# Kernel optimization log

Hardware: AMD Instinct MI355X
Metric: run time of the kernel (lower is better)

## Reference

```python
import jax, jax.numpy as jnp
import numpy as np

E = 2        # expan_att_chans
HEADS = 16   # num_chans * expan_att_chans


def _gconv1x1(x, w, b, groups):
    # Grouped 1x1 conv. x: [B, Cin, H, W]; w: [Cout, Cin//groups]; b: [Cout].
    # Output channel layout matches torch: group-major (c_group * gout + o).
    B, Cin, H, W = x.shape
    Cout = w.shape[0]
    gin, gout = Cin // groups, Cout // groups
    y = jnp.einsum('bgip,goi->bgop',
                   x.reshape(B, groups, gin, H * W),
                   w.reshape(groups, gout, gin))
    return y.reshape(B, Cout, H, W) + b[None, :, None, None]


def _l2norm(x, eps=1e-12):
    # F.normalize(dim=-1): x / max(||x||_2, eps)
    n = jnp.sqrt(jnp.sum(x * x, axis=-1, keepdims=True))
    return x / jnp.maximum(n, eps)


def setup_inputs() -> dict:
    key = jax.random.key(0)
    ks = jax.random.split(key, 12)
    B, C, H, W = 8, 128, 128, 128
    s = 0.05  # small init (module uses xavier gain=0.01)
    f32 = jnp.float32
    return {
        'x': jax.random.normal(ks[0], (B, C, H, W), f32),
        'to': jax.random.normal(ks[1], (B, C, H, W), f32),
        't': jnp.ones((1, HEADS, 1, 1), f32),
        # rgb qkv chain (fusion): C -> 2EC -> EC -> EC, all groups=C
        'w_r1': (jax.random.normal(ks[2], (C * E * 2, 1), f32) * s),
        'b_r1': jnp.zeros((C * E * 2,), f32),
        'w_r2': (jax.random.normal(ks[3], (C * E, 2 * E), f32) * s),
        'b_r2': jnp.zeros((C * E,), f32),
        'w_r3': (jax.random.normal(ks[4], (C * E, E), f32) * s),
        'b_r3': jnp.zeros((C * E,), f32),
        # text kv chain: C -> 2EC -> EC -> 2EC, all groups=C
        'w_t1': (jax.random.normal(ks[5], (C * E * 2, 1), f32) * s),
        'b_t1': jnp.zeros((C * E * 2,), f32),
        'w_t2': (jax.random.normal(ks[6], (C * E, 2 * E), f32) * s),
        'b_t2': jnp.zeros((C * E,), f32),
        'w_t3': (jax.random.normal(ks[7], (C * E * 2, E), f32) * s),
        'b_t3': jnp.zeros((C * E * 2,), f32),
        # fusion conv: Conv2d(E*C -> C, k=3, stride=1, pad=1) + LeakyReLU(0.2)
        'w_f': (jax.random.normal(ks[8], (C, C * E, 3, 3), f32) * 0.02),
        'b_f': jnp.zeros((C,), f32),
    }


def reference(x, to, t, w_r1, b_r1, w_r2, b_r2, w_r3, b_r3,
              w_t1, b_t1, w_t2, b_t2, w_t3, b_t3, w_f, b_f):
    B, C, H, W = x.shape
    Cexp = E * C
    d = Cexp // HEADS  # per-head channel dim
    HW = H * W

    # grouped 1x1 conv chains producing Q (from rgb) and K,V (from text)
    q = _gconv1x1(_gconv1x1(_gconv1x1(x, w_r1, b_r1, C), w_r2, b_r2, C), w_r3, b_r3, C)      # [B, EC, H, W]
    kv = _gconv1x1(_gconv1x1(_gconv1x1(to, w_t1, b_t1, C), w_t2, b_t2, C), w_t3, b_t3, C)    # [B, 2EC, H, W]

    # Rearrange 'B (C E) H W -> B E C H W' then view as [B, heads, d, HW]
    q = q.reshape(B, C, E, HW).transpose(0, 2, 1, 3).reshape(B, HEADS, d, HW)
    kv = kv.reshape(B, C, 2 * E, HW).transpose(0, 2, 1, 3)  # [B, 2E, C, HW]
    k = kv[:, :E].reshape(B, HEADS, d, HW)
    v = kv[:, E:].reshape(B, HEADS, d, HW)

    # channel (transposed) attention with L2-normalized Q,K and learned temperature
    qn, kn = _l2norm(q), _l2norm(k)
    attn = jax.nn.softmax(jnp.einsum('bhdp,bhep->bhde', qn, kn) * t, axis=-1)  # [B, H, d, d]
    xo = jnp.einsum('bhde,bhep->bhdp', attn, v)  # [B, heads, d, HW]

    # rearrange 'B C X (H W) -> B (X C) H W' with C=heads, X=d  (d-major, head-minor)
    xo = xo.transpose(0, 2, 1, 3).reshape(B, Cexp, H, W)

    # group_fus: 3x3 conv (stride 1, pad 1) + LeakyReLU(0.2), residual add
    y = jax.lax.conv_general_dilated(
        xo, w_f, window_strides=(1, 1), padding=((1, 1), (1, 1)),
        dimension_numbers=('NCHW', 'OIHW', 'NCHW'))
    y = jax.nn.leaky_relu(y + b_f[None, :, None, None], negative_slope=0.2)
    return x + y
```

## Files before the change

kernel.cpp:

```cpp
#include <hip/hip_runtime.h>
#include <math.h>

#define B_  8
#define C_  128
#define H_  128
#define W_  128
#define HW_ 16384

#define OFF_MPART 0
#define OFF_SPART 262144
#define OFF_M     327680
#define OFF_S     344064
#define OFF_WV    348160
#define OFF_CST   380928
#define OFF_T     382976
#define OFF_WEFF  392192
#define OFF_T2F   982016
#define T2_ROW    16640
#define T2_BATCH  2163200
#define WS_NEED   (982016ull * 4ull + 34611200ull)

typedef __attribute__((ext_vector_type(8))) short short8;
typedef __attribute__((ext_vector_type(4))) float f32x4;

__device__ __forceinline__ unsigned short f2bf(float f) {
  unsigned u = __float_as_uint(f);
  u += 0x7fffu + ((u >> 16) & 1u);
  return (unsigned short)(u >> 16);
}

__device__ __forceinline__ f32x4 mfma16(short8 a, short8 b, f32x4 c) {
  return __builtin_amdgcn_mfma_f32_16x16x32_bf16(a, b, c, 0, 0, 0);
}

__device__ __forceinline__ void gl16(const void* g, void* l) {
  const unsigned loff = (unsigned)(unsigned long long)l;
  __builtin_amdgcn_global_load_lds(
      (const __attribute__((address_space(1))) void*)g,
      (__attribute__((address_space(3))) void*)loff, 16, 0, 0);
}

__global__ __launch_bounds__(256) void k_gram(const float* __restrict__ x,
                                              const float* __restrict__ to,
                                              float* __restrict__ ws) {
  const int bid = blockIdx.x;
  const int ps  = bid & 15;
  const int blk = (bid >> 4) & 7;
  const int b   = bid >> 7;
  const int tid = threadIdx.x;
  const int w = tid >> 6, l = tid & 63;
  const int lm = l & 15, lh = l >> 4;
  const int c0 = blk * 16;

  const float* xc = x  + ((size_t)b * C_ + c0 + lm) * HW_;
  const float* tc = to + ((size_t)b * C_ + c0 + lm) * HW_;
  const int p0 = ps * 1024 + w * 256 + lh * 8;

  f32x4 acc = (f32x4)0.f;
  float sx = 0.f, sxx = 0.f, st = 0.f, stt = 0.f;
#pragma unroll
  for (int it = 0; it < 8; ++it) {
    const int p = p0 + it * 32;
    const f32x4 xa = *(const f32x4*)(xc + p);
    const f32x4 xb = *(const f32x4*)(xc + p + 4);
    const f32x4 ta = *(const f32x4*)(tc + p);
    const f32x4 tb = *(const f32x4*)(tc + p + 4);
    short8 xf, tf;
#pragma unroll
    for (int e = 0; e < 4; ++e) {
      xf[e]     = (short)f2bf(xa[e]);
      xf[4 + e] = (short)f2bf(xb[e]);
      tf[e]     = (short)f2bf(ta[e]);
      tf[4 + e] = (short)f2bf(tb[e]);
      sx += xa[e] + xb[e];
      sxx = fmaf(xa[e], xa[e], fmaf(xb[e], xb[e], sxx));
      st += ta[e] + tb[e];
      stt = fmaf(ta[e], ta[e], fmaf(tb[e], tb[e], stt));
    }
    acc = mfma16(xf, tf, acc);
  }

  sx  += __shfl_xor(sx, 16);  sx  += __shfl_xor(sx, 32);
  sxx += __shfl_xor(sxx, 16); sxx += __shfl_xor(sxx, 32);
  st  += __shfl_xor(st, 16);  st  += __shfl_xor(st, 32);
  stt += __shfl_xor(stt, 16); stt += __shfl_xor(stt, 32);

  __shared__ float smM[4][256];
  __shared__ float smS[4][4][16];
#pragma unroll
  for (int r = 0; r < 4; ++r)
    smM[w][(lh * 4 + r) * 16 + lm] = acc[r];
  if (l < 16) {
    smS[w][0][lm] = sx;  smS[w][1][lm] = sxx;
    smS[w][2][lm] = st;  smS[w][3][lm] = stt;
  }
  __syncthreads();

  {
    const float s = smM[0][tid & 255] + smM[1][tid & 255]
                  + smM[2][tid & 255] + smM[3][tid & 255];
    ws[OFF_MPART + (size_t)((b * 8 + blk) * 16 + ps) * 256 + tid] = s;
  }
  if (tid < 64) {
    const int kind = tid >> 4, ch = tid & 15;
    const float s = smS[0][kind][ch] + smS[1][kind][ch]
                  + smS[2][kind][ch] + smS[3][kind][ch];
    ws[OFF_SPART + (size_t)kind * 16384 + (size_t)(b * C_ + c0 + ch) * 16 + ps] = s;
  }
}

__global__ __launch_bounds__(256) void k_redB(float* __restrict__ ws) {
  const int gid = blockIdx.x * 256 + threadIdx.x;
  if (gid < 16384) {
    const float* mp = ws + OFF_MPART + (size_t)(gid >> 8) * 4096 + (gid & 255);
    float s = 0.f;
#pragma unroll
    for (int kc = 0; kc < 16; ++kc) s += mp[kc * 256];
    ws[OFF_M + gid] = s;
  } else {
    const int sidx = gid - 16384;
    const float* sp = ws + OFF_SPART + (size_t)sidx * 16;
    float s = 0.f;
#pragma unroll
    for (int kc = 0; kc < 16; ++kc) s += sp[kc];
    ws[OFF_S + sidx] = s;
  }
}

__global__ __launch_bounds__(256) void k_zero(unsigned short* __restrict__ t2) {
  const int b = blockIdx.x >> 1, r = blockIdx.x & 1;
  unsigned short* row = t2 + (size_t)b * T2_BATCH + (size_t)(r ? 129 : 0) * T2_ROW;
  const short8 z = {0,0,0,0,0,0,0,0};
  for (int idx = threadIdx.x; idx < 2080; idx += 256)
    *(short8*)(row + (size_t)idx * 8) = z;
}

__global__ __launch_bounds__(256) void k_tr(const float* __restrict__ to,
                                            unsigned short* __restrict__ t2) {
  const int d  = blockIdx.x;
  const int xh = d & 1;
  const int y  = (d >> 1) & 127;
  const int b  = d >> 8;
  const int tid = threadIdx.x;
  __shared__ char lds[64 * 256];

  const int x0 = xh * 64;
  const int xq = tid & 15;
  const int cg = tid >> 4;
  const float* srcb = to + ((size_t)b * C_ + cg * 8) * HW_ + (size_t)y * W_ + x0 + xq * 4;
#pragma unroll
  for (int k = 0; k < 8; ++k) {
    const f32x4 v = *(const f32x4*)(srcb + (size_t)k * HW_);
    const int c = cg * 8 + k;
#pragma unroll
    for (int e = 0; e < 4; ++e) {
      const int xl = xq * 4 + e;
      const int boff = xl * 256 + ((2 * c) ^ ((xl & 7) << 4));
      *(unsigned short*)(lds + boff) = f2bf(v[e]);
    }
  }
  __syncthreads();

  unsigned short* rowbase = t2 + (size_t)b * T2_BATCH + (size_t)(y + 1) * T2_ROW;
#pragma unroll
  for (int i = 0; i < 4; ++i) {
    const int xx = tid >> 2;
    const int cs = (tid & 3) + i * 4;
    short8 val = *(short8*)(lds + xx * 256 + ((cs * 16) ^ ((xx & 7) << 4)));
    *(short8*)(rowbase + (size_t)(x0 + xx + 1) * 128 + cs * 8) = val;
  }
  if (tid < 16) {
    short8 z = {0,0,0,0,0,0,0,0};
    if (xh == 0) *(short8*)(rowbase + tid * 8) = z;
    else         *(short8*)(rowbase + (size_t)129 * 128 + tid * 8) = z;
  }
}

__global__ __launch_bounds__(256) void k_attn(const float* __restrict__ t,
    const float* __restrict__ w_r1, const float* __restrict__ b_r1,
    const float* __restrict__ w_r2, const float* __restrict__ b_r2,
    const float* __restrict__ w_r3, const float* __restrict__ b_r3,
    const float* __restrict__ w_t1, const float* __restrict__ b_t1,
    const float* __restrict__ w_t2, const float* __restrict__ b_t2,
    const float* __restrict__ w_t3, const float* __restrict__ b_t3,
    float* __restrict__ ws) {
  const int b = blockIdx.x;
  const int tid = threadIdx.x;
  __shared__ float aQ[256], bQ[256], aK[256], bK[256], aV[256], bV[256];
  __shared__ float rks[256], kAs[256], kBs[256], stos[256];

  if (tid < 128) {
    const int g = tid;
    float A1[4], B1[4], A2[2], B2[2];
#pragma unroll
    for (int j = 0; j < 4; ++j) { A1[j] = w_r1[g * 4 + j]; B1[j] = b_r1[g * 4 + j]; }
#pragma unroll
    for (int i = 0; i < 2; ++i) {
      A2[i] = 0.f; B2[i] = b_r2[g * 2 + i];
#pragma unroll
      for (int j = 0; j < 4; ++j) {
        const float w = w_r2[(g * 2 + i) * 4 + j];
        A2[i] = fmaf(w, A1[j], A2[i]); B2[i] = fmaf(w, B1[j], B2[i]);
      }
    }
#pragma unroll
    for (int o = 0; o < 2; ++o) {
      float a = 0.f, bb = b_r3[g * 2 + o];
#pragma unroll
      for (int i = 0; i < 2; ++i) {
        const float w = w_r3[(g * 2 + o) * 2 + i];
        a = fmaf(w, A2[i], a); bb = fmaf(w, B2[i], bb);
      }
      aQ[g * 2 + o] = a; bQ[g * 2 + o] = bb;
    }
#pragma unroll
    for (int j = 0; j < 4; ++j) { A1[j] = w_t1[g * 4 + j]; B1[j] = b_t1[g * 4 + j]; }
#pragma unroll
    for (int i = 0; i < 2; ++i) {
      A2[i] = 0.f; B2[i] = b_t2[g * 2 + i];
#pragma unroll
      for (int j = 0; j < 4; ++j) {
        const float w = w_t2[(g * 2 + i) * 4 + j];
        A2[i] = fmaf(w, A1[j], A2[i]); B2[i] = fmaf(w, B1[j], B2[i]);
      }
    }
#pragma unroll
    for (int o = 0; o < 4; ++o) {
      float a = 0.f, bb = b_t3[g * 4 + o];
#pragma unroll
      for (int i = 0; i < 2; ++i) {
        const float w = w_t3[(g * 4 + o) * 2 + i];
        a = fmaf(w, A2[i], a); bb = fmaf(w, B2[i], bb);
      }
      if (o < 2) { aK[g * 2 + o] = a; bK[g * 2 + o] = bb; }
      else       { aV[g * 2 + (o - 2)] = a; bV[g * 2 + (o - 2)] = bb; }
    }
  }
  __syncthreads();

  const float* S   = ws + OFF_S;
  const float* Sx  = S;
  const float* Sxx = S + 1024;
  const float* Sto = S + 2048;
  const float* Stt = S + 3072;

  {
    const int h = tid >> 4, e = h >> 3, blk = h & 7, c0 = blk * 16;
    const int g = c0 + (tid & 15);
    const float a = aK[g * 2 + e], bb = bK[g * 2 + e];
    const float s2 = a * a * Stt[b * C_ + g] + 2.f * a * bb * Sto[b * C_ + g]
                   + bb * bb * 16384.f;
    rks[tid] = 1.f / fmaxf(sqrtf(fmaxf(s2, 0.f)), 1e-12f);
    kAs[tid] = a; kBs[tid] = bb;
    stos[tid] = Sto[b * C_ + g];
  }
  __syncthreads();

  {
    const int h = tid >> 4, i = tid & 15, e = h >> 3, blk = h & 7, c0 = blk * 16;
    const int gi = c0 + i;
    const float gA = aQ[gi * 2 + e], gB = bQ[gi * 2 + e];
    const float sxi = Sx[b * C_ + gi];
    const float q2 = gA * gA * Sxx[b * C_ + gi] + 2.f * gA * gB * sxi
                   + gB * gB * 16384.f;
    const float rnq = 1.f / fmaxf(sqrtf(fmaxf(q2, 0.f)), 1e-12f);
    const float tt = t[h];
    const float* Mrow = ws + OFF_M + (size_t)(b * 8 + blk) * 256 + i * 16;

    float lg[16];
    float mx = -1e30f;
#pragma unroll
    for (int j = 0; j < 16; ++j) {
      const float s = gA * kAs[h * 16 + j] * Mrow[j]
                    + gA * kBs[h * 16 + j] * sxi
                    + gB * kAs[h * 16 + j] * stos[h * 16 + j]
                    + gB * kBs[h * 16 + j] * 16384.f;
      const float l = tt * s * rnq * rks[h * 16 + j];
      lg[j] = l;
      mx = fmaxf(mx, l);
    }
    float den = 0.f;
#pragma unroll
    for (int j = 0; j < 16; ++j) { const float ev = expf(lg[j] - mx); lg[j] = ev; den += ev; }
    const float inv = 1.f / den;
    float cs = 0.f;
    float* WVp = ws + OFF_WV + (size_t)(b * 16 + h) * 256 + i * 16;
#pragma unroll
    for (int j = 0; j < 16; ++j) {
      const float aa = lg[j] * inv;
      const int gj = c0 + j;
      WVp[j] = aa * aV[gj * 2 + e];
      cs = fmaf(aa, bV[gj * 2 + e], cs);
    }
    ws[OFF_CST + b * 256 + i * 16 + h] = cs;
  }
}

__global__ __launch_bounds__(128) void k_weff(const float* __restrict__ w_f,
                                              float* __restrict__ ws) {
  const int b = blockIdx.x >> 7, oc = blockIdx.x & 127;
  const int c = threadIdx.x, blk = c >> 4, j = c & 15;
  const float* WVb = ws + OFF_WV;
  float acc[9];
#pragma unroll
  for (int k = 0; k < 9; ++k) acc[k] = 0.f;
#pragma unroll
  for (int e = 0; e < 2; ++e) {
    const int h = e * 8 + blk;
#pragma unroll
    for (int i = 0; i < 16; ++i) {
      const float coef = WVb[((size_t)(b * 16 + h) * 16 + i) * 16 + j];
      const float* wf = w_f + (size_t)(oc * 256 + i * 16 + h) * 9;
#pragma unroll
      for (int k = 0; k < 9; ++k) acc[k] = fmaf(wf[k], coef, acc[k]);
    }
  }
  unsigned short* wb16 = (unsigned short*)(ws + OFF_WEFF);
#pragma unroll
  for (int k = 0; k < 9; ++k)
    wb16[(((size_t)(b * 9 + k)) * 128 + oc) * 128 + c] = f2bf(acc[k]);

  __shared__ float tp[9][128];
  float tl[9];
#pragma unroll
  for (int k = 0; k < 9; ++k) tl[k] = 0.f;
  const float* cst = ws + OFF_CST + b * 256;
  for (int cc = c; cc < 256; cc += 128) {
    const float cv = cst[cc];
    const float* wf = w_f + (size_t)(oc * 256 + cc) * 9;
#pragma unroll
    for (int k = 0; k < 9; ++k) tl[k] = fmaf(wf[k], cv, tl[k]);
  }
#pragma unroll
  for (int k = 0; k < 9; ++k) tp[k][c] = tl[k];
  __syncthreads();
  for (int s = 64; s > 0; s >>= 1) {
    if (c < s) {
#pragma unroll
      for (int k = 0; k < 9; ++k) tp[k][c] += tp[k][c + s];
    }
    __syncthreads();
  }
  if (c < 9) ws[OFF_T + ((size_t)b * 128 + oc) * 9 + c] = tp[c][0];
}

__global__ __launch_bounds__(256, 2) void k_conv(const float* __restrict__ xin,
                                                 const float* __restrict__ b_f,
                                                 const float* __restrict__ ws,
                                                 const unsigned short* __restrict__ t2,
                                                 float* __restrict__ out) {
  const int d = blockIdx.x;
  const int b = d & 7;
  const int y = d >> 3;
  const int tid = threadIdx.x;

  __shared__ unsigned short As[2][128 * 64];
  __shared__ unsigned short Bs[2][128 * 64];

  const unsigned short* wb = (const unsigned short*)(ws + OFF_WEFF)
      + (size_t)b * 9 * 16384;
  const unsigned short* t2y = t2 + (size_t)b * T2_BATCH + (size_t)y * T2_ROW;

  const int l = tid & 63;
  const int lm = l & 15, lh = l >> 4;
  const int wv = tid >> 6;
  const int oc0w = (wv & 1) * 64;
  const int px0w = (wv >> 1) * 64;

  const int trow0 = tid >> 3, tci0 = tid & 7;
  const unsigned udstw = (unsigned)((tid & ~63) * 16);

#define STAGE(BUF, S)                                                          \
  {                                                                            \
    const int tap_ = (S) >> 1, ks_ = (S) & 1;                                  \
    const int dy_ = tap_ / 3, dx_ = tap_ - dy_ * 3;                            \
    const unsigned short* asrc = wb + (size_t)tap_ * 16384 + ks_ * 64;         \
    const unsigned short* bsrc = t2y + (size_t)dy_ * T2_ROW + dx_ * 128 + ks_ * 64; \
    _Pragma("unroll")                                                          \
    for (int k_ = 0; k_ < 4; ++k_) {                                           \
      const int row_ = k_ * 32 + trow0;                                        \
      const unsigned dst_ = (unsigned)(k_ * 4096) + udstw;                     \
      const size_t soff_ = (size_t)row_ * 128 + ((tci0 ^ (row_ & 7)) << 3);    \
      gl16(asrc + soff_, (char*)&As[BUF][0] + dst_);                           \
      gl16(bsrc + soff_, (char*)&Bs[BUF][0] + dst_);                           \
    }                                                                          \
  }

  f32x4 acc[4][4];
#pragma unroll
  for (int mt = 0; mt < 4; ++mt)
#pragma unroll
    for (int nt = 0; nt < 4; ++nt) acc[mt][nt] = (f32x4)0.f;

  STAGE(0, 0);
  __syncthreads();

  int cur = 0;
#pragma unroll 1
  for (int s = 0; s < 18; ++s) {
    if (s + 1 < 18) STAGE(cur ^ 1, s + 1);

    const char* Ab = (const char*)&As[cur][0];
    const char* Bb = (const char*)&Bs[cur][0];
#pragma unroll
    for (int ki = 0; ki < 2; ++ki) {
      short8 af[4], bfr[4];
#pragma unroll
      for (int mt = 0; mt < 4; ++mt) {
        const int oc = oc0w + mt * 16 + lm;
        af[mt] = *(const short8*)(Ab + oc * 128 + (((ki * 4 + lh) ^ (oc & 7)) << 4));
      }
#pragma unroll
      for (int nt = 0; nt < 4; ++nt) {
        const int px = px0w + nt * 16 + lm;
        bfr[nt] = *(const short8*)(Bb + px * 128 + (((ki * 4 + lh) ^ (px & 7)) << 4));
      }
#pragma unroll
      for (int mt = 0; mt < 4; ++mt) {
        acc[mt][0] = mfma16(af[mt], bfr[0], acc[mt][0]);
        acc[mt][1] = mfma16(af[mt], bfr[1], acc[mt][1]);
        acc[mt][2] = mfma16(af[mt], bfr[2], acc[mt][2]);
        acc[mt][3] = mfma16(af[mt], bfr[3], acc[mt][3]);
      }
    }
    __syncthreads();
    cur ^= 1;
  }
#undef STAGE

  float* sm = (float*)&As[0][0];
  if (tid < 128) {
    const float* Tk = ws + OFF_T + (size_t)(b * 128 + tid) * 9;
    float s = Tk[3] + Tk[4] + Tk[5], sl = Tk[3], sr = Tk[5];
    if (y >= 1)   { s += Tk[0] + Tk[1] + Tk[2]; sl += Tk[0]; sr += Tk[2]; }
    if (y <= 126) { s += Tk[6] + Tk[7] + Tk[8]; sl += Tk[6]; sr += Tk[8]; }
    sm[tid] = s + b_f[tid]; sm[128 + tid] = sl; sm[256 + tid] = sr;
  }
  __syncthreads();

#pragma unroll
  for (int mt = 0; mt < 4; ++mt)
#pragma unroll
    for (int nt = 0; nt < 4; ++nt) {
      const int px = px0w + nt * 16 + lm;
#pragma unroll
      for (int r = 0; r < 4; ++r) {
        const int oc = oc0w + mt * 16 + lh * 4 + r;
        float add = sm[oc];
        if (px == 0)   add -= sm[128 + oc];
        if (px == 127) add -= sm[256 + oc];
        const float z = acc[mt][nt][r] + add;
        const size_t base = ((size_t)(b * C_ + oc)) * HW_ + (size_t)y * W_ + px;
        const float rx = xin[base];
        out[base] = rx + (z >= 0.f ? z : 0.2f * z);
      }
    }
}

__global__ __launch_bounds__(512, 4) void k_conv_fb(const float* __restrict__ xin,
                                                    const float* __restrict__ to,
                                                    const float* __restrict__ b_f,
                                                    const float* __restrict__ ws,
                                                    float* __restrict__ out) {
  const int bid = blockIdx.x;
  const int nb  = (bid & 7) * 128 + (bid >> 3);
  const int b   = nb >> 7;
  const int y   = nb & 127;
  const int tid = threadIdx.x;

  __shared__ f32x4 ldsbuf[3120];
  char* lp = (char*)ldsbuf;

  f32x4 acc[4][2];
#pragma unroll
  for (int mt = 0; mt < 4; ++mt)
#pragma unroll
    for (int nt = 0; nt < 2; ++nt) acc[mt][nt] = (f32x4)0.f;

  const float* tob = to + (size_t)b * C_ * HW_;
  const unsigned short* wb16 =
      (const unsigned short*)(ws + OFF_WEFF) + (size_t)b * 9 * 128 * 128;

  const int l = tid & 63, wv = tid >> 6;
  const int ocb0 = (wv & 1) * 64, pxb0 = (wv >> 1) * 32;
  const int lm = l & 15, lh = l >> 4;

  for (int cb = 0; cb < 128; cb += 64) {
    __syncthreads();
    {
      const int xg = tid & 31, cq = (tid >> 5) & 15;
      const int cbase = cb + cq * 4;
#pragma unroll
      for (int row = 0; row < 3; ++row) {
        const int y_in = y + row - 1;
        const bool yok = ((unsigned)y_in < 128u);
        const float* src = tob + (size_t)cbase * HW_ + (size_t)y_in * W_;
#pragma unroll
        for (int xb = 0; xb < 5; ++xb) {
          const int xi = xb * 32 + xg;
          if (xi < 130) {
            const int x_in = xi - 1;
            const bool ok = yok && ((unsigned)x_in < 128u);
            float f0 = 0.f, f1 = 0.f, f2 = 0.f, f3 = 0.f;
            if (ok) {
              f0 = src[x_in];
              f1 = src[HW_ + x_in];
              f2 = src[2 * HW_ + x_in];
              f3 = src[3 * HW_ + x_in];
            }
            ushort4 pk;
            pk.x = f2bf(f0); pk.y = f2bf(f1); pk.z = f2bf(f2); pk.w = f2bf(f3);
            const int boff = (row * 130 + xi) * 128 + ((cq * 8) ^ ((xi & 7) << 4));
            *(ushort4*)(lp + boff) = pk;
          }
        }
      }
    }
    __syncthreads();

    for (int tap = 0; tap < 9; ++tap) {
      const int dy = tap / 3, dx = tap - dy * 3;
#pragma unroll
      for (int ks = 0; ks < 2; ++ks) {
        short8 bfr[2];
#pragma unroll
        for (int nt = 0; nt < 2; ++nt) {
          const int xi = pxb0 + nt * 16 + lm + dx;
          const int boff = (dy * 130 + xi) * 128 + ((ks * 64 + lh * 16) ^ ((xi & 7) << 4));
          bfr[nt] = *(const short8*)(lp + boff);
        }
        const int cin = cb + ks * 32 + lh * 8;
#pragma unroll
        for (int mt = 0; mt < 4; ++mt) {
          const int oc = ocb0 + mt * 16 + lm;
          const short8 af = *(const short8*)(wb16 + ((size_t)tap * 128 + oc) * 128 + cin);
          acc[mt][0] = mfma16(af, bfr[0], acc[mt][0]);
          acc[mt][1] = mfma16(af, bfr[1], acc[mt][1]);
        }
      }
    }
  }

  __syncthreads();
  float* sAdd = (float*)ldsbuf;
  float* sLft = sAdd + 128;
  float* sRgt = sAdd + 256;
  if (tid < 128) {
    const float* Tk = ws + OFF_T + (size_t)(b * 128 + tid) * 9;
    float s = Tk[3] + Tk[4] + Tk[5], sl = Tk[3], sr = Tk[5];
    if (y >= 1)   { s += Tk[0] + Tk[1] + Tk[2]; sl += Tk[0]; sr += Tk[2]; }
    if (y <= 126) { s += Tk[6] + Tk[7] + Tk[8]; sl += Tk[6]; sr += Tk[8]; }
    sAdd[tid] = s + b_f[tid]; sLft[tid] = sl; sRgt[tid] = sr;
  }
  __syncthreads();

#pragma unroll
  for (int mt = 0; mt < 4; ++mt)
#pragma unroll
    for (int nt = 0; nt < 2; ++nt) {
      const int px = pxb0 + nt * 16 + lm;
#pragma unroll
      for (int r = 0; r < 4; ++r) {
        const int oc = ocb0 + mt * 16 + lh * 4 + r;
        float add = sAdd[oc];
        if (px == 0)   add -= sLft[oc];
        if (px == 127) add -= sRgt[oc];
        const float z = acc[mt][nt][r] + add;
        const size_t base = ((size_t)(b * C_ + oc)) * HW_ + (size_t)y * W_ + px;
        const float rx = xin[base];
        out[base] = rx + (z >= 0.f ? z : 0.2f * z);
      }
    }
}

extern "C" void kernel_launch(void* const* d_in, const int* in_sizes, int n_in,
                              void* d_out, int out_size, void* d_ws, size_t ws_size,
                              hipStream_t stream) {
  (void)in_sizes; (void)n_in; (void)out_size;
  const float* x    = (const float*)d_in[0];
  const float* to   = (const float*)d_in[1];
  const float* t    = (const float*)d_in[2];
  const float* w_r1 = (const float*)d_in[3];
  const float* b_r1 = (const float*)d_in[4];
  const float* w_r2 = (const float*)d_in[5];
  const float* b_r2 = (const float*)d_in[6];
  const float* w_r3 = (const float*)d_in[7];
  const float* b_r3 = (const float*)d_in[8];
  const float* w_t1 = (const float*)d_in[9];
  const float* b_t1 = (const float*)d_in[10];
  const float* w_t2 = (const float*)d_in[11];
  const float* b_t2 = (const float*)d_in[12];
  const float* w_t3 = (const float*)d_in[13];
  const float* b_t3 = (const float*)d_in[14];
  const float* w_f  = (const float*)d_in[15];
  const float* b_f  = (const float*)d_in[16];
  float* ws  = (float*)d_ws;
  float* out = (float*)d_out;
  unsigned short* t2 = (unsigned short*)(ws + OFF_T2F);
  const bool fast = (ws_size >= WS_NEED);

  k_gram<<<1024, 256, 0, stream>>>(x, to, ws);
  k_redB<<<80, 256, 0, stream>>>(ws);
  if (fast) {
    k_zero<<<16, 256, 0, stream>>>(t2);
    k_tr<<<2048, 256, 0, stream>>>(to, t2);
  }
  k_attn<<<8, 256, 0, stream>>>(t, w_r1, b_r1, w_r2, b_r2, w_r3, b_r3,
                                w_t1, b_t1, w_t2, b_t2, w_t3, b_t3, ws);
  k_weff<<<1024, 128, 0, stream>>>(w_f, ws);
  if (fast) k_conv<<<1024, 256, 0, stream>>>(x, b_f, ws, t2, out);
  else      k_conv_fb<<<1024, 512, 0, stream>>>(x, to, b_f, ws, out);
}
```

Measured before the change: 114.5 us.

## Compute two output rows per conv block with a shared four-row input halo tile

The implicit-GEMM 3x3 conv now has each 512-thread block compute two output rows. It loads a four-row padded input halo (one K half at a time) into LDS once and reuses it across all nine taps, instead of restaging a shifted input tile for every tap. Only the weight tile is double-buffered per tap, which cuts global/L2 traffic for the activation operand. In exchange the block uses about 82 KB of LDS, lowering occupancy, and the halo load is not overlapped with compute at each K-half boundary.

```diff
diff --git a/kernel.cpp b/kernel.cpp
--- a/kernel.cpp
+++ b/kernel.cpp
@@ -344,46 +344,66 @@
   if (c < 9) ws[OFF_T + ((size_t)b * 128 + oc) * 9 + c] = tp[c][0];
 }
 
-__global__ __launch_bounds__(256, 2) void k_conv(const float* __restrict__ xin,
+__global__ __launch_bounds__(512, 2) void k_conv(const float* __restrict__ xin,
                                                  const float* __restrict__ b_f,
                                                  const float* __restrict__ ws,
                                                  const unsigned short* __restrict__ t2,
                                                  float* __restrict__ out) {
-  const int d = blockIdx.x;
-  const int b = d & 7;
-  const int y = d >> 3;
+  const int d  = blockIdx.x;
+  const int b  = d & 7;
+  const int y2 = d >> 3;
   const int tid = threadIdx.x;
 
-  __shared__ unsigned short As[2][128 * 64];
-  __shared__ unsigned short Bs[2][128 * 64];
+  __shared__ unsigned short B4s[33280];
+  __shared__ unsigned short As[2][8192];
 
   const unsigned short* wb = (const unsigned short*)(ws + OFF_WEFF)
       + (size_t)b * 9 * 16384;
-  const unsigned short* t2y = t2 + (size_t)b * T2_BATCH + (size_t)y * T2_ROW;
+  const unsigned short* t2b4 = t2 + (size_t)b * T2_BATCH
+      + (size_t)(y2 * 2) * T2_ROW;
 
   const int l = tid & 63;
   const int lm = l & 15, lh = l >> 4;
   const int wv = tid >> 6;
   const int oc0w = (wv & 1) * 64;
-  const int px0w = (wv >> 1) * 64;
-
-  const int trow0 = tid >> 3, tci0 = tid & 7;
+  const int px0w = ((wv >> 1) & 1) * 64;
+  const int rw   = wv >> 2;
+
   const unsigned udstw = (unsigned)((tid & ~63) * 16);
 
-#define STAGE(BUF, S)                                                          \
+#define STAGE_B4(KS)                                                           \
   {                                                                            \
-    const int tap_ = (S) >> 1, ks_ = (S) & 1;                                  \
-    const int dy_ = tap_ / 3, dx_ = tap_ - dy_ * 3;                            \
-    const unsigned short* asrc = wb + (size_t)tap_ * 16384 + ks_ * 64;         \
-    const unsigned short* bsrc = t2y + (size_t)dy_ * T2_ROW + dx_ * 128 + ks_ * 64; \
     _Pragma("unroll")                                                          \
-    for (int k_ = 0; k_ < 4; ++k_) {                                           \
-      const int row_ = k_ * 32 + trow0;                                        \
-      const unsigned dst_ = (unsigned)(k_ * 4096) + udstw;                     \
-      const size_t soff_ = (size_t)row_ * 128 + ((tci0 ^ (row_ & 7)) << 3);    \
-      gl16(asrc + soff_, (char*)&As[BUF][0] + dst_);                           \
-      gl16(bsrc + soff_, (char*)&Bs[BUF][0] + dst_);                           \
+    for (int i_ = 0; i_ < 8; ++i_) {                                           \
+      const int q_ = i_ * 512 + tid;                                           \
+      const int rr_ = q_ / 1040;                                               \
+      const int rem_ = q_ - rr_ * 1040;                                        \
+      const int xi_ = rem_ >> 3, c8_ = rem_ & 7;                               \
+      gl16(t2b4 + (size_t)rr_ * T2_ROW + xi_ * 128 + (KS) * 64                 \
+               + ((c8_ ^ (xi_ & 7)) << 3),                                     \
+           (char*)B4s + (unsigned)(i_ * 8192) + udstw);                        \
     }                                                                          \
+    if (tid < 64) {                                                            \
+      const int q_ = 4096 + tid;                                               \
+      const int rr_ = q_ / 1040;                                               \
+      const int rem_ = q_ - rr_ * 1040;                                        \
+      const int xi_ = rem_ >> 3, c8_ = rem_ & 7;                               \
+      gl16(t2b4 + (size_t)rr_ * T2_ROW + xi_ * 128 + (KS) * 64                 \
+               + ((c8_ ^ (xi_ & 7)) << 3),                                     \
+           (char*)B4s + 65536u);                                               \
+    }                                                                          \
+  }
+
+#define STAGE_A(BUF, TAP, KS)                                                  \
+  {                                                                            \
+    const unsigned short* asrc = wb + (size_t)(TAP) * 16384 + (KS) * 64;       \
+    _Pragma("unroll")                                                          \
+    for (int k_ = 0; k_ < 2; ++k_) {                                           \
+      const int task_ = k_ * 512 + tid;                                        \
+      const int trow_ = task_ >> 3, c8_ = task_ & 7;                           \
+      gl16(asrc + (size_t)trow_ * 128 + ((c8_ ^ (trow_ & 7)) << 3),            \
+           (char*)&As[BUF][0] + (unsigned)(k_ * 8192) + udstw);                \
+    }                                                                          \
   }
 
   f32x4 acc[4][4];
@@ -392,52 +412,65 @@
 #pragma unroll
     for (int nt = 0; nt < 4; ++nt) acc[mt][nt] = (f32x4)0.f;
 
-  STAGE(0, 0);
-  __syncthreads();
-
-  int cur = 0;
 #pragma unroll 1
-  for (int s = 0; s < 18; ++s) {
-    if (s + 1 < 18) STAGE(cur ^ 1, s + 1);
-
-    const char* Ab = (const char*)&As[cur][0];
-    const char* Bb = (const char*)&Bs[cur][0];
-#pragma unroll
-    for (int ki = 0; ki < 2; ++ki) {
-      short8 af[4], bfr[4];
-#pragma unroll
-      for (int mt = 0; mt < 4; ++mt) {
-        const int oc = oc0w + mt * 16 + lm;
-        af[mt] = *(const short8*)(Ab + oc * 128 + (((ki * 4 + lh) ^ (oc & 7)) << 4));
-      }
-#pragma unroll
-      for (int nt = 0; nt < 4; ++nt) {
-        const int px = px0w + nt * 16 + lm;
-        bfr[nt] = *(const short8*)(Bb + px * 128 + (((ki * 4 + lh) ^ (px & 7)) << 4));
-      }
-#pragma unroll
-      for (int mt = 0; mt < 4; ++mt) {
-        acc[mt][0] = mfma16(af[mt], bfr[0], acc[mt][0]);
-        acc[mt][1] = mfma16(af[mt], bfr[1], acc[mt][1]);
-        acc[mt][2] = mfma16(af[mt], bfr[2], acc[mt][2]);
-        acc[mt][3] = mfma16(af[mt], bfr[3], acc[mt][3]);
-      }
-    }
+  for (int ks = 0; ks < 2; ++ks) {
+    STAGE_B4(ks);
+    STAGE_A(0, 0, ks);
     __syncthreads();
-    cur ^= 1;
-  }
-#undef STAGE
-
-  float* sm = (float*)&As[0][0];
-  if (tid < 128) {
-    const float* Tk = ws + OFF_T + (size_t)(b * 128 + tid) * 9;
+
+    int cur = 0;
+#pragma unroll 1
+    for (int tap = 0; tap < 9; ++tap) {
+      if (tap + 1 < 9) STAGE_A(cur ^ 1, tap + 1, ks);
+
+      const int dy = tap / 3, dx = tap - dy * 3;
+      const int rdy = rw + dy;
+      const char* Ab = (const char*)&As[cur][0];
+      const char* Bb = (const char*)B4s;
+#pragma unroll
+      for (int ki = 0; ki < 2; ++ki) {
+        short8 af[4], bfr[4];
+#pragma unroll
+        for (int mt = 0; mt < 4; ++mt) {
+          const int oc = oc0w + mt * 16 + lm;
+          af[mt] = *(const short8*)(Ab + oc * 128 + (((ki * 4 + lh) ^ (oc & 7)) << 4));
+        }
+#pragma unroll
+        for (int nt = 0; nt < 4; ++nt) {
+          const int xi = px0w + nt * 16 + lm + dx;
+          bfr[nt] = *(const short8*)(Bb + (rdy * 130 + xi) * 128
+                                        + (((ki * 4 + lh) ^ (xi & 7)) << 4));
+        }
+#pragma unroll
+        for (int mt = 0; mt < 4; ++mt) {
+          acc[mt][0] = mfma16(af[mt], bfr[0], acc[mt][0]);
+          acc[mt][1] = mfma16(af[mt], bfr[1], acc[mt][1]);
+          acc[mt][2] = mfma16(af[mt], bfr[2], acc[mt][2]);
+          acc[mt][3] = mfma16(af[mt], bfr[3], acc[mt][3]);
+        }
+      }
+      __syncthreads();
+      cur ^= 1;
+    }
+  }
+#undef STAGE_A
+#undef STAGE_B4
+
+  float* sm = (float*)B4s;
+  if (tid < 256) {
+    const int rr = tid >> 7, oc = tid & 127;
+    const int y = y2 * 2 + rr;
+    const float* Tk = ws + OFF_T + (size_t)(b * 128 + oc) * 9;
     float s = Tk[3] + Tk[4] + Tk[5], sl = Tk[3], sr = Tk[5];
     if (y >= 1)   { s += Tk[0] + Tk[1] + Tk[2]; sl += Tk[0]; sr += Tk[2]; }
     if (y <= 126) { s += Tk[6] + Tk[7] + Tk[8]; sl += Tk[6]; sr += Tk[8]; }
-    sm[tid] = s + b_f[tid]; sm[128 + tid] = sl; sm[256 + tid] = sr;
-  }
-  __syncthreads();
-
+    sm[rr * 384 + oc] = s + b_f[oc];
+    sm[rr * 384 + 128 + oc] = sl;
+    sm[rr * 384 + 256 + oc] = sr;
+  }
+  __syncthreads();
+
+  const int y = y2 * 2 + rw;
 #pragma unroll
   for (int mt = 0; mt < 4; ++mt)
 #pragma unroll
@@ -446,9 +479,9 @@
 #pragma unroll
       for (int r = 0; r < 4; ++r) {
         const int oc = oc0w + mt * 16 + lh * 4 + r;
-        float add = sm[oc];
-        if (px == 0)   add -= sm[128 + oc];
-        if (px == 127) add -= sm[256 + oc];
+        float add = sm[rw * 384 + oc];
+        if (px == 0)   add -= sm[rw * 384 + 128 + oc];
+        if (px == 127) add -= sm[rw * 384 + 256 + oc];
         const float z = acc[mt][nt][r] + add;
         const size_t base = ((size_t)(b * C_ + oc)) * HW_ + (size_t)y * W_ + px;
         const float rx = xin[base];
@@ -608,6 +641,6 @@
   k_attn<<<8, 256, 0, stream>>>(t, w_r1, b_r1, w_r2, b_r2, w_r3, b_r3,
                                 w_t1, b_t1, w_t2, b_t2, w_t3, b_t3, ws);
   k_weff<<<1024, 128, 0, stream>>>(w_f, ws);
-  if (fast) k_conv<<<1024, 256, 0, stream>>>(x, b_f, ws, t2, out);
+  if (fast) k_conv<<<512, 512, 0, stream>>>(x, b_f, ws, t2, out);
   else      k_conv_fb<<<1024, 512, 0, stream>>>(x, to, b_f, ws, out);
 }
```

New measurement: 114.6 us. Within noise of the previous version (+0.0%).
